# Kernel optimization log

Hardware: AMD Instinct MI355X
Metric: run time of the kernel (lower is better)

The kernel has to match this reference:

```python
import jax, jax.numpy as jnp
import numpy as np

B, C, H, G1, G2 = 16, 64, 128, 64, 64  # batch, input channels, hidden, grid dims


def setup_inputs() -> dict:
    key = jax.random.key(0)
    ks = jax.random.split(key, 5)
    s = 0.05  # small init to keep gates in a sane range
    return {
        "x": jax.random.normal(ks[0], (B, C, G1, G2), jnp.float32),
        "W_ih": jax.random.normal(ks[1], (2, 4 * H, C), jnp.float32) * s,
        "W_hh": jax.random.normal(ks[2], (2, 4 * H, 2 * H), jnp.float32) * s,
        "b_ih": jax.random.normal(ks[3], (2, 4 * H), jnp.float32) * s,
        "b_hh": jax.random.normal(ks[4], (2, 4 * H), jnp.float32) * s,
    }


def _lstm_update(gates, c_prev):
    # PyTorch LSTMCell gate order: i, f, g, o
    i, f, g, o = jnp.split(gates, 4, axis=-1)
    c = jax.nn.sigmoid(f) * c_prev + jax.nn.sigmoid(i) * jnp.tanh(g)
    h = jax.nn.sigmoid(o) * jnp.tanh(c)
    return h, c


def _grid_lstm(x, W_ih, W_hh, b_ih, b_hh):
    Bn = x.shape[0]
    Hn = W_hh.shape[1] // 4
    g2 = x.shape[3]
    # Precompute the input contribution to the gates for every grid location
    # (no recurrence on x). xg: [2(dim), G1, G2, B, 4H]
    xg = jnp.einsum('bcij,dgc->dijbg', x, W_ih) \
        + (b_ih + b_hh)[:, None, None, None, :]
    Wh0t = W_hh[0].T  # [2H, 4H]
    Wh1t = W_hh[1].T  # [2H, 4H]
    z = jnp.zeros((Bn, Hn), x.dtype)
    zrow = jnp.zeros((g2, Bn, Hn), x.dtype)

    def col_step(carry, xs):
        # recurrence along grid dim 1 (columns)
        h2, c2 = carry                # dim-1 state from (i, j-1): [B, H]
        xg0, xg1, h1p, c1p = xs       # dim-0 state from (i-1, j)
        Hcat = jnp.concatenate([h1p, h2], axis=-1)  # [B, 2H] shared hidden
        h1n, c1n = _lstm_update(xg0 + Hcat @ Wh0t, c1p)
        h2n, c2n = _lstm_update(xg1 + Hcat @ Wh1t, c2)
        return (h2n, c2n), (h1n, c1n, h2n)

    def row_step(carry, xg_row):
        # recurrence along grid dim 0 (rows); carry = dim-0 state of prev row
        h1_row, c1_row = carry        # [G2, B, H]
        _, (h1s, c1s, h2s) = jax.lax.scan(
            col_step, (z, z), (xg_row[0], xg_row[1], h1_row, c1_row))
        return (h1s, c1s), (h1s, h2s)

    xg_rows = jnp.moveaxis(xg, 1, 0)  # [G1, 2, G2, B, 4H]
    _, (h1_all, h2_all) = jax.lax.scan(row_step, (zrow, zrow), xg_rows)
    # h*_all: [G1, G2, B, H]; concat hidden of all dims along channel
    out = jnp.concatenate([h1_all, h2_all], axis=-1)  # [G1, G2, B, 2H]
    return out.transpose(2, 3, 0, 1)                  # [B, 2H, G1, G2]


def reference(x, W_ih, W_hh, b_ih, b_hh):
    return _grid_lstm(x, W_ih, W_hh, b_ih, b_hh)
```

## Files before the change

### kernel.cpp

```cpp
#include <hip/hip_runtime.h>
#include <math.h>

namespace {

constexpr int BN = 16;
constexpr int CN = 64;
constexpr int HN = 128;
constexpr int GN = 64;
constexpr int KH = 2 * HN;
constexpr int KTOT = KH + CN;
constexpr int LDSK = 328;
constexpr int GBS2 = 260;

typedef _Float16 half8 __attribute__((ext_vector_type(8)));
typedef float float4v __attribute__((ext_vector_type(4)));
typedef unsigned long long u64;

__device__ __forceinline__ float fsig(float z) {
    return 1.f / (1.f + expf(-z));
}

__global__ __launch_bounds__(256) void prep_kernel(
    const float* __restrict__ Wih,
    const float* __restrict__ Whh,
    _Float16* __restrict__ wf,
    const float* __restrict__ x,
    _Float16* __restrict__ xb)
{
    const int blk = blockIdx.x;
    if (blk < 640) {
        const int t = threadIdx.x;
        if (t < 64) {
            const int nt = blk / 10, ks = blk - nt * 10;
            const int lane = t;
            const int dd = nt >> 5;
            const int gr = (nt & 31) * 16 + (lane & 15);
            const int k0 = ks * 32 + (lane >> 4) * 8;
            _Float16* dst = wf + ((size_t)blk * 64 + lane) * 8;
            #pragma unroll
            for (int e = 0; e < 8; ++e) {
                const int k = k0 + e;
                const float v = (k < KH)
                    ? Whh[((size_t)(dd * 512 + gr)) * KH + k]
                    : Wih[((size_t)(dd * 512 + gr)) * CN + (k - KH)];
                dst[e] = (_Float16)v;
            }
        }
    } else {
        __shared__ float tile[CN][GN + 1];
        const int bb = blk - 640;
        const int b = bb >> 6;
        const int i = bb & 63;
        const int t = threadIdx.x;
        const int tj = t & 63, tc = t >> 6;
        for (int c0 = 0; c0 < CN; c0 += 4) {
            const int c = c0 + tc;
            tile[c][tj] = x[((size_t)(b * CN + c) * GN + i) * GN + tj];
        }
        __syncthreads();
        const int wc = t & 63, wj = t >> 6;
        for (int j0 = 0; j0 < GN; j0 += 4) {
            const int j = j0 + wj;
            xb[((size_t)(i * GN + j) * BN + b) * CN + wc] = (_Float16)tile[wc][j];
        }
    }
}

__global__ __launch_bounds__(256) void out_kernel(
    const _Float16* __restrict__ hbuf, float* __restrict__ out)
{
    const int b = blockIdx.x >> 6;
    const int i = blockIdx.x & 63;
    const int t = threadIdx.x;
    float* op = out + ((size_t)(b * KH + t)) * (GN * GN) + (size_t)i * GN;
    const _Float16* hp = hbuf + ((size_t)i * GN * BN + b) * KH + t;
    #pragma unroll 4
    for (int j = 0; j < GN; ++j)
        op[j] = (float)hp[(size_t)j * (BN * KH)];
}

template <bool USE_XB>
__global__ __launch_bounds__(512, 1) void grid_lstm_rowq(
    const _Float16* __restrict__ wf,
    const _Float16* __restrict__ xb,
    const float* __restrict__ x,
    const float* __restrict__ bih,
    const float* __restrict__ bhh,
    _Float16* __restrict__ hbuf,
    float* __restrict__ cmail,
    int* __restrict__ flag1,
    int* __restrict__ flag2)
{
    __shared__ __align__(16) _Float16 Wl2[16 * 8 * 64 * 8];
    __shared__ __align__(16) _Float16 Hc[BN * LDSK];
    __shared__ __align__(16) float gb[BN * GBS2];
    __shared__ float blds[256];

    const int blk = blockIdx.x;
    const int i  = blk & 63;
    const int s  = blk >> 6;
    const int dd = s >> 1;
    const int ub = s & 1;

    const int t = threadIdx.x;
    const int lane = t & 63;
    const int wv = t >> 6;
    const int l15 = lane & 15;
    const int l4 = lane >> 4;

    const half8* wfv = (const half8*)wf;
    half8* wl2v = (half8*)Wl2;

    for (int e = t; e < 16 * 8 * 64; e += 512) {
        const int ln = e & 63, ks = (e >> 6) & 7, tl = e >> 9;
        const int q = tl >> 2, w = tl & 3;
        const int nt = dd * 32 + q * 8 + ub * 4 + w;
        wl2v[e] = wfv[(size_t)(nt * 10 + ks) * 64 + ln];
    }
    const int tlA = 2 * wv, tlB = 2 * wv + 1;
    const int ntA = dd * 32 + (tlA >> 2) * 8 + ub * 4 + (tlA & 3);
    const int ntB = dd * 32 + (tlB >> 2) * 8 + ub * 4 + (tlB & 3);
    const half8 wA8 = wfv[(size_t)(ntA * 10 + 8) * 64 + lane];
    const half8 wA9 = wfv[(size_t)(ntA * 10 + 9) * 64 + lane];
    const half8 wB8 = wfv[(size_t)(ntB * 10 + 8) * 64 + lane];
    const half8 wB9 = wfv[(size_t)(ntB * 10 + 9) * 64 + lane];
    if (t < 256) {
        const int q = t >> 6, uu = t & 63;
        const int gr = dd * 512 + q * 128 + ub * 64 + uu;
        blds[t] = bih[gr] + bhh[gr];
    }
    const int sb = (t & 255) >> 4;
    const int sk = (t & 15);
    const bool roleH1 = (t < 256);
    const int eb = t >> 5;
    const int u2 = (t & 31) * 2;
    float c2r0 = 0.f, c2r1 = 0.f;

    if (USE_XB) {
        if (t < 256)
            *(u64*)(&Hc[(t >> 4) * LDSK + KH + (t & 15) * 4]) =
                *(const u64*)(xb + ((size_t)(i * GN)) * (BN * CN)
                              + (t >> 4) * CN + (t & 15) * 4);
    } else {
        #pragma unroll
        for (int r = 0; r < 2; ++r) {
            const int e = t + r * 512;
            const int b2 = e >> 6, c = e & 63;
            Hc[b2 * LDSK + KH + c] =
                (_Float16)x[(size_t)(b2 * 64 + c) * 4096 + i * 64];
        }
    }
    __syncthreads();

    for (int j = 0; j < GN; ++j) {
        const int cellidx = i * GN + j;

        {
            u64 q0 = 0, q1 = 0;
            if (roleH1) {
                if (i > 0) {
                    const int* fp = flag1 + cellidx - GN;
                    int it = 0;
                    while (__hip_atomic_load(fp, __ATOMIC_RELAXED,
                                             __HIP_MEMORY_SCOPE_AGENT) < 2) {
                        __builtin_amdgcn_s_sleep(1);
                        if (++it > (1 << 24)) break;
                    }
                    const u64* src = (const u64*)(hbuf
                        + ((size_t)(cellidx - GN)) * (BN * KH) + sb * KH + sk * 8);
                    q0 = __hip_atomic_load(src, __ATOMIC_RELAXED,
                                           __HIP_MEMORY_SCOPE_AGENT);
                    q1 = __hip_atomic_load(src + 1, __ATOMIC_RELAXED,
                                           __HIP_MEMORY_SCOPE_AGENT);
                }
                *(u64*)(&Hc[sb * LDSK + sk * 8]) = q0;
                *(u64*)(&Hc[sb * LDSK + sk * 8 + 4]) = q1;
            } else {
                if (j > 0) {
                    const int* fp = flag2 + cellidx - 1;
                    int it = 0;
                    while (__hip_atomic_load(fp, __ATOMIC_RELAXED,
                                             __HIP_MEMORY_SCOPE_AGENT) < 2) {
                        __builtin_amdgcn_s_sleep(1);
                        if (++it > (1 << 24)) break;
                    }
                    const u64* src = (const u64*)(hbuf
                        + ((size_t)(cellidx - 1)) * (BN * KH)
                        + sb * KH + HN + sk * 8);
                    q0 = __hip_atomic_load(src, __ATOMIC_RELAXED,
                                           __HIP_MEMORY_SCOPE_AGENT);
                    q1 = __hip_atomic_load(src + 1, __ATOMIC_RELAXED,
                                           __HIP_MEMORY_SCOPE_AGENT);
                }
                *(u64*)(&Hc[sb * LDSK + HN + sk * 8]) = q0;
                *(u64*)(&Hc[sb * LDSK + HN + sk * 8 + 4]) = q1;
            }
        }
        __syncthreads();

        {
            half8 a[10];
            #pragma unroll
            for (int ks = 0; ks < 10; ++ks)
                a[ks] = *(const half8*)(&Hc[l15 * LDSK + ks * 32 + l4 * 8]);
            float4v acc0 = {0.f, 0.f, 0.f, 0.f};
            float4v acc1 = {0.f, 0.f, 0.f, 0.f};
            #pragma unroll
            for (int ks = 0; ks < 8; ++ks) {
                acc0 = __builtin_amdgcn_mfma_f32_16x16x32_f16(
                    a[ks], wl2v[(tlA * 8 + ks) * 64 + lane], acc0, 0, 0, 0);
                acc1 = __builtin_amdgcn_mfma_f32_16x16x32_f16(
                    a[ks], wl2v[(tlB * 8 + ks) * 64 + lane], acc1, 0, 0, 0);
            }
            acc0 = __builtin_amdgcn_mfma_f32_16x16x32_f16(a[8], wA8, acc0, 0, 0, 0);
            acc0 = __builtin_amdgcn_mfma_f32_16x16x32_f16(a[9], wA9, acc0, 0, 0, 0);
            acc1 = __builtin_amdgcn_mfma_f32_16x16x32_f16(a[8], wB8, acc1, 0, 0, 0);
            acc1 = __builtin_amdgcn_mfma_f32_16x16x32_f16(a[9], wB9, acc1, 0, 0, 0);
            #pragma unroll
            for (int rg = 0; rg < 4; ++rg) {
                gb[(l4 * 4 + rg) * GBS2 + tlA * 16 + l15] = acc0[rg];
                gb[(l4 * 4 + rg) * GBS2 + tlB * 16 + l15] = acc1[rg];
            }
        }
        __syncthreads();

        u64 xv = 0;
        const bool doX = USE_XB && (t < 256) && (j + 1 < GN);
        if (doX)
            xv = *(const u64*)(xb + ((size_t)(cellidx + 1)) * (BN * CN)
                               + (t >> 4) * CN + (t & 15) * 4);

        {
            float g0[4], g1[4];
            #pragma unroll
            for (int q = 0; q < 4; ++q) {
                g0[q] = gb[eb * GBS2 + q * 64 + u2]     + blds[q * 64 + u2];
                g1[q] = gb[eb * GBS2 + q * 64 + u2 + 1] + blds[q * 64 + u2 + 1];
            }
            const int hu = ub * 64 + u2;
            float cp0, cp1;
            if (dd == 0) {
                cp0 = 0.f; cp1 = 0.f;
                if (i > 0) {
                    const u64 cq = __hip_atomic_load(
                        (const u64*)(cmail + ((size_t)((((i - 1) & 1) * GN + j) * BN
                                     + eb)) * HN + hu),
                        __ATOMIC_RELAXED, __HIP_MEMORY_SCOPE_AGENT);
                    union { u64 q; float f[2]; } cu; cu.q = cq;
                    cp0 = cu.f[0]; cp1 = cu.f[1];
                }
            } else {
                cp0 = c2r0; cp1 = c2r1;
            }
            const float c0 = fsig(g0[1]) * cp0 + fsig(g0[0]) * tanhf(g0[2]);
            const float c1 = fsig(g1[1]) * cp1 + fsig(g1[0]) * tanhf(g1[2]);
            const float h0 = fsig(g0[3]) * tanhf(c0);
            const float h1 = fsig(g1[3]) * tanhf(c1);
            union { unsigned int u; _Float16 f[2]; } hp;
            hp.f[0] = (_Float16)h0; hp.f[1] = (_Float16)h1;

            if (dd == 0) {
                union { u64 q; float f[2]; } cn; cn.f[0] = c0; cn.f[1] = c1;
                __hip_atomic_store(
                    (u64*)(cmail + ((size_t)(((i & 1) * GN + j) * BN + eb)) * HN + hu),
                    cn.q, __ATOMIC_RELAXED, __HIP_MEMORY_SCOPE_AGENT);
            } else {
                c2r0 = c0; c2r1 = c1;
            }
            __hip_atomic_store(
                (unsigned int*)(hbuf + ((size_t)cellidx) * (BN * KH)
                                + eb * KH + dd * HN + hu),
                hp.u, __ATOMIC_RELAXED, __HIP_MEMORY_SCOPE_AGENT);
        }

        if (doX)
            *(u64*)(&Hc[(t >> 4) * LDSK + KH + (t & 15) * 4]) = xv;
        if (!USE_XB && (j + 1 < GN)) {
            #pragma unroll
            for (int r = 0; r < 2; ++r) {
                const int e = t + r * 512;
                const int b2 = e >> 6, c = e & 63;
                Hc[b2 * LDSK + KH + c] =
                    (_Float16)x[(size_t)(b2 * 64 + c) * 4096 + i * 64 + (j + 1)];
            }
        }

        asm volatile("s_waitcnt vmcnt(0)" ::: "memory");
        __syncthreads();
        if (t == 0)
            __hip_atomic_fetch_add((dd == 0 ? flag1 : flag2) + cellidx, 1,
                                   __ATOMIC_RELAXED, __HIP_MEMORY_SCOPE_AGENT);
    }
}

constexpr int KCH = 32;
constexpr int NCH = KTOT / KCH;

__device__ __forceinline__ float sigmoidf_(float z) {
    return 1.f / (1.f + expf(-z));
}

__global__ __launch_bounds__(256, 1) void diag_kernel(
    const float* __restrict__ x, const float* __restrict__ Wih,
    const float* __restrict__ Whh, const float* __restrict__ bih,
    const float* __restrict__ bhh, float* __restrict__ out,
    float* __restrict__ cbuf, int d)
{
    __shared__ float HcF[BN][KTOT];
    __shared__ float Wch[KCH][257];
    const int cell = blockIdx.x >> 2;
    const int slice = blockIdx.x & 3;
    const int dd = slice >> 1;
    const int h0 = (slice & 1) * 64;
    const int i0 = (d > GN - 1) ? (d - (GN - 1)) : 0;
    const int i = i0 + cell;
    const int j = d - i;
    const int t = threadIdx.x;
    for (int e = t; e < BN * KTOT; e += 256) {
        const int b = e / KTOT, k = e - b * KTOT;
        float v;
        if (k < HN)      v = (i > 0) ? out[((b * KH + k) * GN + (i - 1)) * GN + j] : 0.f;
        else if (k < KH) v = (j > 0) ? out[((b * KH + k) * GN + i) * GN + (j - 1)] : 0.f;
        else             v = x[((b * CN + (k - KH)) * GN + i) * GN + j];
        HcF[b][k] = v;
    }
    const int h = t & 63, bg = t >> 6;
    const int grow = dd * 4 * HN + bg * HN + h0 + h;
    float acc[4][4];
    #pragma unroll
    for (int qq = 0; qq < 4; ++qq)
        #pragma unroll
        for (int bb = 0; bb < 4; ++bb) acc[qq][bb] = 0.f;
    for (int kb = 0; kb < NCH; ++kb) {
        const int kbase = kb * KCH;
        __syncthreads();
        const float* src = (kbase < KH) ? (Whh + (size_t)grow * KH + kbase)
                                        : (Wih + (size_t)grow * CN + (kbase - KH));
        #pragma unroll
        for (int k4 = 0; k4 < KCH / 4; ++k4) {
            const float4 w = *(const float4*)(src + k4 * 4);
            Wch[k4 * 4 + 0][t] = w.x; Wch[k4 * 4 + 1][t] = w.y;
            Wch[k4 * 4 + 2][t] = w.z; Wch[k4 * 4 + 3][t] = w.w;
        }
        __syncthreads();
        #pragma unroll 8
        for (int kk = 0; kk < KCH; ++kk) {
            const float w0 = Wch[kk][0 * 64 + h], w1 = Wch[kk][1 * 64 + h];
            const float w2 = Wch[kk][2 * 64 + h], w3 = Wch[kk][3 * 64 + h];
            #pragma unroll
            for (int bb = 0; bb < 4; ++bb) {
                const float hv = HcF[bg * 4 + bb][kbase + kk];
                acc[0][bb] = fmaf(w0, hv, acc[0][bb]);
                acc[1][bb] = fmaf(w1, hv, acc[1][bb]);
                acc[2][bb] = fmaf(w2, hv, acc[2][bb]);
                acc[3][bb] = fmaf(w3, hv, acc[3][bb]);
            }
        }
    }
    const int hu = h0 + h;
    float bias[4];
    #pragma unroll
    for (int qq = 0; qq < 4; ++qq) {
        const int gidx = dd * 4 * HN + qq * HN + hu;
        bias[qq] = bih[gidx] + bhh[gidx];
    }
    float* cptr = (dd == 0) ? (cbuf + (size_t)j * BN * HN)
                            : (cbuf + (size_t)GN * BN * HN + (size_t)i * BN * HN);
    const bool has_prev = (dd == 0) ? (i > 0) : (j > 0);
    #pragma unroll
    for (int bb = 0; bb < 4; ++bb) {
        const int b = bg * 4 + bb;
        const float gi = sigmoidf_(acc[0][bb] + bias[0]);
        const float gf = sigmoidf_(acc[1][bb] + bias[1]);
        const float gg = tanhf(acc[2][bb] + bias[2]);
        const float go = sigmoidf_(acc[3][bb] + bias[3]);
        const float cp = has_prev ? cptr[b * HN + hu] : 0.f;
        const float c = gf * cp + gi * gg;
        cptr[b * HN + hu] = c;
        out[((b * KH + dd * HN + hu) * GN + i) * GN + j] = go * tanhf(c);
    }
}

}

extern "C" void kernel_launch(void* const* d_in, const int* in_sizes, int n_in,
                              void* d_out, int out_size, void* d_ws, size_t ws_size,
                              hipStream_t stream) {
    const float* x   = (const float*)d_in[0];
    const float* Wih = (const float*)d_in[1];
    const float* Whh = (const float*)d_in[2];
    const float* bih = (const float*)d_in[3];
    const float* bhh = (const float*)d_in[4];
    float* out = (float*)d_out;

    const size_t HB_BYTES = (size_t)GN * GN * BN * KH * 2;
    const size_t WF_BYTES = (size_t)640 * 64 * 8 * 2;
    const size_t CM_BYTES = (size_t)2 * GN * BN * HN * 4;
    const size_t FL_BYTES = (size_t)GN * GN * 4;
    const size_t XB_BYTES = (size_t)GN * GN * BN * CN * 2;
    const size_t NEED_MIN  = HB_BYTES + WF_BYTES + CM_BYTES + 2 * FL_BYTES;
    const size_t NEED_FULL = NEED_MIN + XB_BYTES;

    if (ws_size >= NEED_MIN) {
        char* p = (char*)d_ws;
        _Float16* hbuf  = (_Float16*)p;                 p += HB_BYTES;
        _Float16* wfp   = (_Float16*)p;                 p += WF_BYTES;
        float*    cmail = (float*)p;                    p += CM_BYTES;
        int*      flag1 = (int*)p;                      p += FL_BYTES;
        int*      flag2 = (int*)p;                      p += FL_BYTES;
        _Float16* xbp   = (_Float16*)p;

        hipMemsetAsync(flag1, 0, 2 * FL_BYTES, stream);

        if (ws_size >= NEED_FULL) {
            hipLaunchKernelGGL(prep_kernel, dim3(640 + BN * GN), dim3(256), 0,
                               stream, Wih, Whh, wfp, x, xbp);
            void* args[] = { (void*)&wfp, (void*)&xbp, (void*)&x, (void*)&bih,
                             (void*)&bhh, (void*)&hbuf, (void*)&cmail,
                             (void*)&flag1, (void*)&flag2 };
            hipLaunchCooperativeKernel((const void*)grid_lstm_rowq<true>,
                                       dim3(256), dim3(512), args, 0, stream);
        } else {
            hipLaunchKernelGGL(prep_kernel, dim3(640), dim3(256), 0,
                               stream, Wih, Whh, wfp, x, xbp);
            void* args[] = { (void*)&wfp, (void*)&xbp, (void*)&x, (void*)&bih,
                             (void*)&bhh, (void*)&hbuf, (void*)&cmail,
                             (void*)&flag1, (void*)&flag2 };
            hipLaunchCooperativeKernel((const void*)grid_lstm_rowq<false>,
                                       dim3(256), dim3(512), args, 0, stream);
        }
        hipLaunchKernelGGL(out_kernel, dim3(BN * GN), dim3(256), 0, stream,
                           hbuf, out);
    } else {
        float* cbuf = (float*)d_ws;
        for (int d = 0; d < 2 * GN - 1; ++d) {
            const int i0 = (d > GN - 1) ? (d - (GN - 1)) : 0;
            const int i1 = (d < GN - 1) ? d : (GN - 1);
            const int nc = i1 - i0 + 1;
            hipLaunchKernelGGL(diag_kernel, dim3(nc * 4), dim3(256), 0, stream,
                               x, Wih, Whh, bih, bhh, out, cbuf, d);
        }
    }
}
```

Baseline: 467.4 us.

## Split recurrent GEMM around dependency wait, per-wave flags, fast activations

Each wave now signals completion with its own flag increment, so consumers wait for a count of 16 instead of 2. This drops the end-of-step block barrier. The recurrent matmul is split so the MFMA over the already available row-hidden and input chunks runs before the horizontal-neighbour hidden state is written into LDS. That overlaps part of the compute with the wait on the left cell. Sigmoid and tanh switch to __expf-based approximations, which trades some accuracy for fewer instructions. Removing the barrier risks LDS reuse hazards across iterations.

```diff
diff --git a/kernel.cpp b/kernel.cpp
--- a/kernel.cpp
+++ b/kernel.cpp
@@ -17,7 +17,10 @@
 typedef unsigned long long u64;
 
 __device__ __forceinline__ float fsig(float z) {
-    return 1.f / (1.f + expf(-z));
+    return 1.f / (1.f + __expf(-z));
+}
+__device__ __forceinline__ float ftanh(float z) {
+    return 1.f - 2.f / (__expf(2.f * z) + 1.f);
 }
 
 __global__ __launch_bounds__(256) void prep_kernel(
@@ -155,67 +158,90 @@
     for (int j = 0; j < GN; ++j) {
         const int cellidx = i * GN + j;
 
+        u64 q0 = 0, q1 = 0;
+        if (roleH1) {
+            if (i > 0) {
+                const int* fp = flag1 + cellidx - GN;
+                int it = 0;
+                while (__hip_atomic_load(fp, __ATOMIC_RELAXED,
+                                         __HIP_MEMORY_SCOPE_AGENT) < 16) {
+                    __builtin_amdgcn_s_sleep(1);
+                    if (++it > (1 << 24)) break;
+                }
+                const u64* src = (const u64*)(hbuf
+                    + ((size_t)(cellidx - GN)) * (BN * KH) + sb * KH + sk * 8);
+                q0 = __hip_atomic_load(src, __ATOMIC_RELAXED,
+                                       __HIP_MEMORY_SCOPE_AGENT);
+                q1 = __hip_atomic_load(src + 1, __ATOMIC_RELAXED,
+                                       __HIP_MEMORY_SCOPE_AGENT);
+            }
+            *(u64*)(&Hc[sb * LDSK + sk * 8]) = q0;
+            *(u64*)(&Hc[sb * LDSK + sk * 8 + 4]) = q1;
+        } else {
+            if (j > 0) {
+                const int* fp = flag2 + cellidx - 1;
+                int it = 0;
+                while (__hip_atomic_load(fp, __ATOMIC_RELAXED,
+                                         __HIP_MEMORY_SCOPE_AGENT) < 16) {
+                    __builtin_amdgcn_s_sleep(1);
+                    if (++it > (1 << 24)) break;
+                }
+                const u64* src = (const u64*)(hbuf
+                    + ((size_t)(cellidx - 1)) * (BN * KH)
+                    + sb * KH + HN + sk * 8);
+                q0 = __hip_atomic_load(src, __ATOMIC_RELAXED,
+                                       __HIP_MEMORY_SCOPE_AGENT);
+                q1 = __hip_atomic_load(src + 1, __ATOMIC_RELAXED,
+                                       __HIP_MEMORY_SCOPE_AGENT);
+            } else {
+                *(u64*)(&Hc[sb * LDSK + HN + sk * 8]) = 0ull;
+                *(u64*)(&Hc[sb * LDSK + HN + sk * 8 + 4]) = 0ull;
+            }
+        }
+        __syncthreads();
+
+        float4v acc0 = {0.f, 0.f, 0.f, 0.f};
+        float4v acc1 = {0.f, 0.f, 0.f, 0.f};
         {
-            u64 q0 = 0, q1 = 0;
-            if (roleH1) {
-                if (i > 0) {
-                    const int* fp = flag1 + cellidx - GN;
-                    int it = 0;
-                    while (__hip_atomic_load(fp, __ATOMIC_RELAXED,
-                                             __HIP_MEMORY_SCOPE_AGENT) < 2) {
-                        __builtin_amdgcn_s_sleep(1);
-                        if (++it > (1 << 24)) break;
-                    }
-                    const u64* src = (const u64*)(hbuf
-                        + ((size_t)(cellidx - GN)) * (BN * KH) + sb * KH + sk * 8);
-                    q0 = __hip_atomic_load(src, __ATOMIC_RELAXED,
-                                           __HIP_MEMORY_SCOPE_AGENT);
-                    q1 = __hip_atomic_load(src + 1, __ATOMIC_RELAXED,
-                                           __HIP_MEMORY_SCOPE_AGENT);
-                }
-                *(u64*)(&Hc[sb * LDSK + sk * 8]) = q0;
-                *(u64*)(&Hc[sb * LDSK + sk * 8 + 4]) = q1;
-            } else {
-                if (j > 0) {
-                    const int* fp = flag2 + cellidx - 1;
-                    int it = 0;
-                    while (__hip_atomic_load(fp, __ATOMIC_RELAXED,
-                                             __HIP_MEMORY_SCOPE_AGENT) < 2) {
-                        __builtin_amdgcn_s_sleep(1);
-                        if (++it > (1 << 24)) break;
-                    }
-                    const u64* src = (const u64*)(hbuf
-                        + ((size_t)(cellidx - 1)) * (BN * KH)
-                        + sb * KH + HN + sk * 8);
-                    q0 = __hip_atomic_load(src, __ATOMIC_RELAXED,
-                                           __HIP_MEMORY_SCOPE_AGENT);
-                    q1 = __hip_atomic_load(src + 1, __ATOMIC_RELAXED,
-                                           __HIP_MEMORY_SCOPE_AGENT);
-                }
-                *(u64*)(&Hc[sb * LDSK + HN + sk * 8]) = q0;
-                *(u64*)(&Hc[sb * LDSK + HN + sk * 8 + 4]) = q1;
-            }
+            half8 a0 = *(const half8*)(&Hc[l15 * LDSK + 0 * 32 + l4 * 8]);
+            half8 a1 = *(const half8*)(&Hc[l15 * LDSK + 1 * 32 + l4 * 8]);
+            half8 a2 = *(const half8*)(&Hc[l15 * LDSK + 2 * 32 + l4 * 8]);
+            half8 a3 = *(const half8*)(&Hc[l15 * LDSK + 3 * 32 + l4 * 8]);
+            half8 ax0 = *(const half8*)(&Hc[l15 * LDSK + 8 * 32 + l4 * 8]);
+            half8 ax1 = *(const half8*)(&Hc[l15 * LDSK + 9 * 32 + l4 * 8]);
+            acc0 = __builtin_amdgcn_mfma_f32_16x16x32_f16(a0, wl2v[(tlA*8+0)*64+lane], acc0, 0, 0, 0);
+            acc1 = __builtin_amdgcn_mfma_f32_16x16x32_f16(a0, wl2v[(tlB*8+0)*64+lane], acc1, 0, 0, 0);
+            acc0 = __builtin_amdgcn_mfma_f32_16x16x32_f16(a1, wl2v[(tlA*8+1)*64+lane], acc0, 0, 0, 0);
+            acc1 = __builtin_amdgcn_mfma_f32_16x16x32_f16(a1, wl2v[(tlB*8+1)*64+lane], acc1, 0, 0, 0);
+            acc0 = __builtin_amdgcn_mfma_f32_16x16x32_f16(a2, wl2v[(tlA*8+2)*64+lane], acc0, 0, 0, 0);
+            acc1 = __builtin_amdgcn_mfma_f32_16x16x32_f16(a2, wl2v[(tlB*8+2)*64+lane], acc1, 0, 0, 0);
+            acc0 = __builtin_amdgcn_mfma_f32_16x16x32_f16(a3, wl2v[(tlA*8+3)*64+lane], acc0, 0, 0, 0);
+            acc1 = __builtin_amdgcn_mfma_f32_16x16x32_f16(a3, wl2v[(tlB*8+3)*64+lane], acc1, 0, 0, 0);
+            acc0 = __builtin_amdgcn_mfma_f32_16x16x32_f16(ax0, wA8, acc0, 0, 0, 0);
+            acc0 = __builtin_amdgcn_mfma_f32_16x16x32_f16(ax1, wA9, acc0, 0, 0, 0);
+            acc1 = __builtin_amdgcn_mfma_f32_16x16x32_f16(ax0, wB8, acc1, 0, 0, 0);
+            acc1 = __builtin_amdgcn_mfma_f32_16x16x32_f16(ax1, wB9, acc1, 0, 0, 0);
+        }
+
+        if (!roleH1 && j > 0) {
+            *(u64*)(&Hc[sb * LDSK + HN + sk * 8]) = q0;
+            *(u64*)(&Hc[sb * LDSK + HN + sk * 8 + 4]) = q1;
         }
         __syncthreads();
 
         {
-            half8 a[10];
-            #pragma unroll
-            for (int ks = 0; ks < 10; ++ks)
-                a[ks] = *(const half8*)(&Hc[l15 * LDSK + ks * 32 + l4 * 8]);
-            float4v acc0 = {0.f, 0.f, 0.f, 0.f};
-            float4v acc1 = {0.f, 0.f, 0.f, 0.f};
-            #pragma unroll
-            for (int ks = 0; ks < 8; ++ks) {
-                acc0 = __builtin_amdgcn_mfma_f32_16x16x32_f16(
-                    a[ks], wl2v[(tlA * 8 + ks) * 64 + lane], acc0, 0, 0, 0);
-                acc1 = __builtin_amdgcn_mfma_f32_16x16x32_f16(
-                    a[ks], wl2v[(tlB * 8 + ks) * 64 + lane], acc1, 0, 0, 0);
-            }
-            acc0 = __builtin_amdgcn_mfma_f32_16x16x32_f16(a[8], wA8, acc0, 0, 0, 0);
-            acc0 = __builtin_amdgcn_mfma_f32_16x16x32_f16(a[9], wA9, acc0, 0, 0, 0);
-            acc1 = __builtin_amdgcn_mfma_f32_16x16x32_f16(a[8], wB8, acc1, 0, 0, 0);
-            acc1 = __builtin_amdgcn_mfma_f32_16x16x32_f16(a[9], wB9, acc1, 0, 0, 0);
+            half8 a4 = *(const half8*)(&Hc[l15 * LDSK + 4 * 32 + l4 * 8]);
+            half8 a5 = *(const half8*)(&Hc[l15 * LDSK + 5 * 32 + l4 * 8]);
+            half8 a6 = *(const half8*)(&Hc[l15 * LDSK + 6 * 32 + l4 * 8]);
+            half8 a7 = *(const half8*)(&Hc[l15 * LDSK + 7 * 32 + l4 * 8]);
+            acc0 = __builtin_amdgcn_mfma_f32_16x16x32_f16(a4, wl2v[(tlA*8+4)*64+lane], acc0, 0, 0, 0);
+            acc1 = __builtin_amdgcn_mfma_f32_16x16x32_f16(a4, wl2v[(tlB*8+4)*64+lane], acc1, 0, 0, 0);
+            acc0 = __builtin_amdgcn_mfma_f32_16x16x32_f16(a5, wl2v[(tlA*8+5)*64+lane], acc0, 0, 0, 0);
+            acc1 = __builtin_amdgcn_mfma_f32_16x16x32_f16(a5, wl2v[(tlB*8+5)*64+lane], acc1, 0, 0, 0);
+            acc0 = __builtin_amdgcn_mfma_f32_16x16x32_f16(a6, wl2v[(tlA*8+6)*64+lane], acc0, 0, 0, 0);
+            acc1 = __builtin_amdgcn_mfma_f32_16x16x32_f16(a6, wl2v[(tlB*8+6)*64+lane], acc1, 0, 0, 0);
+            acc0 = __builtin_amdgcn_mfma_f32_16x16x32_f16(a7, wl2v[(tlA*8+7)*64+lane], acc0, 0, 0, 0);
+            acc1 = __builtin_amdgcn_mfma_f32_16x16x32_f16(a7, wl2v[(tlB*8+7)*64+lane], acc1, 0, 0, 0);
             #pragma unroll
             for (int rg = 0; rg < 4; ++rg) {
                 gb[(l4 * 4 + rg) * GBS2 + tlA * 16 + l15] = acc0[rg];
@@ -252,10 +278,10 @@
             } else {
                 cp0 = c2r0; cp1 = c2r1;
             }
-            const float c0 = fsig(g0[1]) * cp0 + fsig(g0[0]) * tanhf(g0[2]);
-            const float c1 = fsig(g1[1]) * cp1 + fsig(g1[0]) * tanhf(g1[2]);
-            const float h0 = fsig(g0[3]) * tanhf(c0);
-            const float h1 = fsig(g1[3]) * tanhf(c1);
+            const float c0 = fsig(g0[1]) * cp0 + fsig(g0[0]) * ftanh(g0[2]);
+            const float c1 = fsig(g1[1]) * cp1 + fsig(g1[0]) * ftanh(g1[2]);
+            const float h0 = fsig(g0[3]) * ftanh(c0);
+            const float h1 = fsig(g1[3]) * ftanh(c1);
             union { unsigned int u; _Float16 f[2]; } hp;
             hp.f[0] = (_Float16)h0; hp.f[1] = (_Float16)h1;
 
@@ -286,8 +312,7 @@
         }
 
         asm volatile("s_waitcnt vmcnt(0)" ::: "memory");
-        __syncthreads();
-        if (t == 0)
+        if ((t & 63) == 0)
             __hip_atomic_fetch_add((dd == 0 ? flag1 : flag2) + cellidx, 1,
                                    __ATOMIC_RELAXED, __HIP_MEMORY_SCOPE_AGENT);
     }
```

Result: no change. 471.6 us (+0.9%).
